# Performance work log

Measured on AMD Instinct MI355X. Metric: run time of the kernel, lower is better.

The kernel has to match this reference:

```python
import jax, jax.numpy as jnp
import numpy as np

L, N, B, S, H = 8, 4, 2, 4096, 256  # layers, sharers, batch, seq, hidden_dim
TAU = 0.5


def _mlp5(x, w1, b1, w2, b2):
    # x: [L,N,B,S,C], w1: [L,C,H], w2: [L,H,H] -> per-layer Linear-ReLU-Linear
    h = jax.nn.relu(jnp.einsum('lnbsc,lch->lnbsh', x, w1) + b1[:, None, None, None, :])
    return jnp.einsum('lnbsh,lhd->lnbsd', h, w2) + b2[:, None, None, None, :]


def _mlp4(x, w1, b1, w2, b2):
    # x: [L,B,S,C], w1: [L,C,H], w2: [L,H,H]
    h = jax.nn.relu(jnp.einsum('lbsc,lch->lbsh', x, w1) + b1[:, None, None, :])
    return jnp.einsum('lbsh,lhd->lbsd', h, w2) + b2[:, None, None, :]


def setup_inputs() -> dict:
    key = jax.random.key(0)
    ks = jax.random.split(key, 26)
    sc = 1.0 / np.sqrt(H)
    sc2 = 1.0 / np.sqrt(2 * H)
    d = {
        'receiver_k': jax.random.normal(ks[0], (L, B, S, H), jnp.float32),
        'receiver_v': jax.random.normal(ks[1], (L, B, S, H), jnp.float32),
        'sharer_k': jax.random.normal(ks[2], (L, N, B, S, H), jnp.float32),
        'sharer_v': jax.random.normal(ks[3], (L, N, B, S, H), jnp.float32),
        'edge_weights': jax.random.uniform(ks[4], (L, N), jnp.float32),
        'alpha': jnp.zeros((L,), jnp.float32),  # layer_gates_alpha init = zeros
        'ak_w1': jax.random.normal(ks[5], (L, H, H), jnp.float32) * sc,
        'ak_b1': jnp.zeros((L, H), jnp.float32),
        'ak_w2': jax.random.normal(ks[6], (L, H, H), jnp.float32) * sc,
        'ak_b2': jnp.zeros((L, H), jnp.float32),
        'av_w1': jax.random.normal(ks[7], (L, H, H), jnp.float32) * sc,
        'av_b1': jnp.zeros((L, H), jnp.float32),
        'av_w2': jax.random.normal(ks[8], (L, H, H), jnp.float32) * sc,
        'av_b2': jnp.zeros((L, H), jnp.float32),
        'fk_w1': jax.random.normal(ks[9], (L, 2 * H, H), jnp.float32) * sc2,
        'fk_b1': jnp.zeros((L, H), jnp.float32),
        'fk_w2': jax.random.normal(ks[10], (L, H, H), jnp.float32) * sc,
        'fk_b2': jnp.zeros((L, H), jnp.float32),
        'fv_w1': jax.random.normal(ks[11], (L, 2 * H, H), jnp.float32) * sc2,
        'fv_b1': jnp.zeros((L, H), jnp.float32),
        'fv_w2': jax.random.normal(ks[12], (L, H, H), jnp.float32) * sc,
        'fv_b2': jnp.zeros((L, H), jnp.float32),
    }
    return d


def reference(receiver_k, receiver_v, sharer_k, sharer_v, edge_weights, alpha,
              ak_w1, ak_b1, ak_w2, ak_b2, av_w1, av_b1, av_w2, av_b2,
              fk_w1, fk_b1, fk_w2, fk_b2, fv_w1, fv_b1, fv_w2, fv_b2):
    gate = jax.nn.sigmoid(alpha / TAU)[:, None, None, None]  # [L,1,1,1]
    # Align each sharer cache per layer
    aligned_k = _mlp5(sharer_k, ak_w1, ak_b1, ak_w2, ak_b2)
    aligned_v = _mlp5(sharer_v, av_w1, av_b1, av_w2, av_b2)
    # Weighted aggregation over sharers, divided by sharer count
    agg_k = jnp.einsum('ln,lnbsh->lbsh', edge_weights, aligned_k) / N
    agg_v = jnp.einsum('ln,lnbsh->lbsh', edge_weights, aligned_v) / N
    # Gated fusion with receiver cache
    delta_k = _mlp4(jnp.concatenate([receiver_k, agg_k], axis=-1), fk_w1, fk_b1, fk_w2, fk_b2)
    delta_v = _mlp4(jnp.concatenate([receiver_v, agg_v], axis=-1), fv_w1, fv_b1, fv_w2, fv_b2)
    fused_k = receiver_k + gate * delta_k
    fused_v = receiver_v + gate * delta_v
    return jnp.stack([fused_k, fused_v])  # [2,L,B,S,H]
```

## Files before the change

### kernel.cpp

```cpp
#include <hip/hip_runtime.h>
#include <hip/hip_bf16.h>


typedef unsigned int  u32;
typedef unsigned short u16;
typedef __attribute__((ext_vector_type(8))) short bf16x8;
typedef __attribute__((ext_vector_type(4))) float f32x4;

#define LL   8
#define NN   4
#define HH   256
#define RPL  8192
#define BM   64
#define ST   (BM * HH)

#define LSTRIDE 655360
#define O_AKW1 0
#define O_AKW2 65536
#define O_AVW1 131072
#define O_AVW2 196608
#define O_FKW1 262144
#define O_FKW2 393216
#define O_FVW1 458752
#define O_FVW2 589824

__device__ __forceinline__ u16 f2bf(float f) {
  return __builtin_bit_cast(u16, __float2bfloat16(f));
}
__device__ __forceinline__ float bf2f(u16 b) {
  u32 u = ((u32)b) << 16;
  return __builtin_bit_cast(float, u);
}
__device__ __forceinline__ float4 ldf4(const float* p) { return *(const float4*)p; }

__global__ __launch_bounds__(256) void prep_wt_k(
    const float* __restrict__ s0, const float* __restrict__ s1,
    const float* __restrict__ s2, const float* __restrict__ s3,
    const float* __restrict__ s4, const float* __restrict__ s5,
    const float* __restrict__ s6, const float* __restrict__ s7,
    u16* __restrict__ wt)
{
  __shared__ float tile[32][33];
  const int mat = blockIdx.z, l = blockIdx.y, t = blockIdx.x;
  const float* src; int off, K;
  switch (mat) {
    case 0: src = s0; off = O_AKW1; K = 256; break;
    case 1: src = s1; off = O_AKW2; K = 256; break;
    case 2: src = s2; off = O_AVW1; K = 256; break;
    case 3: src = s3; off = O_AVW2; K = 256; break;
    case 4: src = s4; off = O_FKW1; K = 512; break;
    case 5: src = s5; off = O_FKW2; K = 256; break;
    case 6: src = s6; off = O_FVW1; K = 512; break;
    default: src = s7; off = O_FVW2; K = 256; break;
  }
  const int ntk = K >> 5;
  if (t >= ntk * 8) return;
  const int tk = t % ntk, tp = t / ntk;
  src += (size_t)l * K * HH;
  u16* dst = wt + (size_t)l * LSTRIDE + off;
  #pragma unroll
  for (int i = 0; i < 4; ++i) {
    int idx = threadIdx.x + i * 256;
    int r = idx >> 5, c = idx & 31;
    tile[r][c] = src[(size_t)(tk * 32 + r) * HH + tp * 32 + c];
  }
  __syncthreads();
  const int pl = threadIdx.x >> 3, kq = threadIdx.x & 7;
  const int p = tp * 32 + pl;
  ushort4 o;
  o.x = f2bf(tile[kq * 4 + 0][pl]);
  o.y = f2bf(tile[kq * 4 + 1][pl]);
  o.z = f2bf(tile[kq * 4 + 2][pl]);
  o.w = f2bf(tile[kq * 4 + 3][pl]);
  *(ushort4*)(dst + (size_t)tk * 8192 + p * 32 + kq * 4) = o;
}

__device__ __forceinline__ void zero24(f32x4 (&a)[2][4]) {
  f32x4 z = {0.f, 0.f, 0.f, 0.f};
  #pragma unroll
  for (int i = 0; i < 2; ++i)
    #pragma unroll
    for (int j = 0; j < 4; ++j) a[i][j] = z;
}

__device__ __forceinline__ void stWrite(u16* dst, const float4& v, int idx) {
  int q = idx >> 6, c = (idx & 63) * 4;
  ushort4 o;
  o.x = f2bf(v.x); o.y = f2bf(v.y);
  o.z = f2bf(v.z); o.w = f2bf(v.w);
  *(ushort4*)(dst + q * HH + (c ^ ((q & 7) << 3))) = o;
}

template<bool STG>
__device__ __forceinline__ void gemm8R(
    f32x4 (&acc)[2][4], const bf16x8 (&ws)[16], const u16* __restrict__ act,
    const float* __restrict__ src, u16* __restrict__ dst,
    int tid, int lr, int g)
{
  float4 slot[8];
  if (STG) {
    #pragma unroll
    for (int c = 0; c < 8; ++c)
      slot[c] = ldf4(src + (size_t)(c * 512 + tid) * 4);
    __builtin_amdgcn_sched_barrier(0);
  }
  #pragma unroll
  for (int kt = 0; kt < 8; ++kt) {
    bf16x8 b[4];
    #pragma unroll
    for (int fq = 0; fq < 4; ++fq) {
      int q = fq * 16 + lr;
      int k = (kt * 32 + g * 8) ^ ((q & 7) << 3);
      b[fq] = *(const bf16x8*)(act + q * HH + k);
    }
    #pragma unroll
    for (int fp = 0; fp < 2; ++fp)
      #pragma unroll
      for (int fq = 0; fq < 4; ++fq)
        acc[fp][fq] = __builtin_amdgcn_mfma_f32_16x16x32_bf16(ws[kt * 2 + fp], b[fq], acc[fp][fq], 0, 0, 0);
  }
  if (STG) {
    __builtin_amdgcn_sched_barrier(0);
    #pragma unroll
    for (int c = 0; c < 8; ++c)
      stWrite(dst, slot[c], c * 512 + tid);
  }
}

template<bool STG>
__device__ __forceinline__ void gemm8S(
    f32x4 (&acc)[2][4], const u16* __restrict__ wtile, const u16* __restrict__ act,
    const float* __restrict__ src, u16* __restrict__ dst,
    int tid, int w, int lr, int g)
{
  const u16* wl = wtile + (w * 32 + lr) * 32 + g * 8;
  bf16x8 a[4][2];
  #pragma unroll
  for (int c = 0; c < 3; ++c)
    #pragma unroll
    for (int fp = 0; fp < 2; ++fp)
      a[c][fp] = *(const bf16x8*)(wl + c * 8192 + fp * 512);
  __builtin_amdgcn_sched_barrier(0x38F);
  float4 slot[8];
  if (STG) {
    #pragma unroll
    for (int c = 0; c < 8; ++c)
      slot[c] = ldf4(src + (size_t)(c * 512 + tid) * 4);
    __builtin_amdgcn_sched_barrier(0);
  }
  #pragma unroll
  for (int kt = 0; kt < 8; ++kt) {
    const int cur = kt & 3;
    if (kt < 5) {
      #pragma unroll
      for (int fp = 0; fp < 2; ++fp)
        a[(kt + 3) & 3][fp] = *(const bf16x8*)(wl + (kt + 3) * 8192 + fp * 512);
    }
    bf16x8 b[4];
    #pragma unroll
    for (int fq = 0; fq < 4; ++fq) {
      int q = fq * 16 + lr;
      int k = (kt * 32 + g * 8) ^ ((q & 7) << 3);
      b[fq] = *(const bf16x8*)(act + q * HH + k);
    }
    #pragma unroll
    for (int fp = 0; fp < 2; ++fp)
      #pragma unroll
      for (int fq = 0; fq < 4; ++fq)
        acc[fp][fq] = __builtin_amdgcn_mfma_f32_16x16x32_bf16(a[cur][fp], b[fq], acc[fp][fq], 0, 0, 0);
  }
  if (STG) {
    __builtin_amdgcn_sched_barrier(0);
    #pragma unroll
    for (int c = 0; c < 8; ++c)
      stWrite(dst, slot[c], c * 512 + tid);
  }
}

__device__ __forceinline__ void stageDirect(u16* dst, const float* __restrict__ src, int tid) {
  #pragma unroll
  for (int i = 0; i < 8; ++i) {
    float4 v = ldf4(src + (size_t)(i * 512 + tid) * 4);
    stWrite(dst, v, i * 512 + tid);
  }
}

template<bool INIT>
__device__ __forceinline__ void hsUpd(
    u16* HS, f32x4 (&acc)[2][4], const float* __restrict__ b1,
    float sn, int w, int lr, int g)
{
  #pragma unroll
  for (int fp = 0; fp < 2; ++fp) {
    int p0 = w * 32 + fp * 16 + g * 4;
    float4 bv = *(const float4*)(b1 + p0);
    #pragma unroll
    for (int fq = 0; fq < 4; ++fq) {
      int q = fq * 16 + lr;
      u16* addr = HS + q * HH + (p0 ^ ((q & 7) << 3));
      float v0 = sn * fmaxf(acc[fp][fq][0] + bv.x, 0.f);
      float v1 = sn * fmaxf(acc[fp][fq][1] + bv.y, 0.f);
      float v2 = sn * fmaxf(acc[fp][fq][2] + bv.z, 0.f);
      float v3 = sn * fmaxf(acc[fp][fq][3] + bv.w, 0.f);
      if (!INIT) {
        ushort4 old = *(ushort4*)addr;
        v0 += bf2f(old.x); v1 += bf2f(old.y);
        v2 += bf2f(old.z); v3 += bf2f(old.w);
      }
      ushort4 o;
      o.x = f2bf(v0); o.y = f2bf(v1);
      o.z = f2bf(v2); o.w = f2bf(v3);
      *(ushort4*)addr = o;
    }
  }
}

__device__ __forceinline__ void epiLds(
    u16* buf, f32x4 (&acc)[2][4], const float* __restrict__ bias,
    float bscale, bool doRelu, int w, int lr, int g)
{
  #pragma unroll
  for (int fp = 0; fp < 2; ++fp) {
    int p0 = w * 32 + fp * 16 + g * 4;
    float4 bv = *(const float4*)(bias + p0);
    #pragma unroll
    for (int fq = 0; fq < 4; ++fq) {
      int q = fq * 16 + lr;
      float v0 = acc[fp][fq][0] + bscale * bv.x;
      float v1 = acc[fp][fq][1] + bscale * bv.y;
      float v2 = acc[fp][fq][2] + bscale * bv.z;
      float v3 = acc[fp][fq][3] + bscale * bv.w;
      if (doRelu) {
        v0 = fmaxf(v0, 0.f); v1 = fmaxf(v1, 0.f);
        v2 = fmaxf(v2, 0.f); v3 = fmaxf(v3, 0.f);
      }
      ushort4 o;
      o.x = f2bf(v0); o.y = f2bf(v1);
      o.z = f2bf(v2); o.w = f2bf(v3);
      *(ushort4*)(buf + q * HH + (p0 ^ ((q & 7) << 3))) = o;
    }
  }
}

__device__ __forceinline__ void epiOut(
    f32x4 (&acc)[2][4], const float* __restrict__ bias,
    const float* __restrict__ recv, float* __restrict__ outp,
    float gate, int w, int lr, int g)
{
  #pragma unroll
  for (int fp = 0; fp < 2; ++fp) {
    int p0 = w * 32 + fp * 16 + g * 4;
    float4 bv = *(const float4*)(bias + p0);
    #pragma unroll
    for (int fq = 0; fq < 4; ++fq) {
      int q = fq * 16 + lr;
      float4 rv = *(const float4*)(recv + (size_t)q * HH + p0);
      float4 ov;
      ov.x = rv.x + gate * (acc[fp][fq][0] + bv.x);
      ov.y = rv.y + gate * (acc[fp][fq][1] + bv.y);
      ov.z = rv.z + gate * (acc[fp][fq][2] + bv.z);
      ov.w = rv.w + gate * (acc[fp][fq][3] + bv.w);
      *(float4*)(outp + (size_t)q * HH + p0) = ov;
    }
  }
}

__global__ __launch_bounds__(512) void CacheFuser_73873437491748_kernel(
    const float* __restrict__ recv_k, const float* __restrict__ recv_v,
    const float* __restrict__ shar_k, const float* __restrict__ shar_v,
    const float* __restrict__ ew, const float* __restrict__ alpha,
    const float* __restrict__ ak_b1, const float* __restrict__ ak_b2,
    const float* __restrict__ av_b1, const float* __restrict__ av_b2,
    const float* __restrict__ fk_b1, const float* __restrict__ fk_b2,
    const float* __restrict__ fv_b1, const float* __restrict__ fv_b2,
    const u16* __restrict__ wt, float* __restrict__ out)
{
  __shared__ u16 XA[ST];
  __shared__ u16 XB[ST];
  __shared__ u16 HS[ST];
  __shared__ u16 FB[ST];

  const int bid = blockIdx.x;
  const int l = bid & 7, t = bid >> 3;
  const int tid = threadIdx.x;
  const int w = tid >> 6, lane = tid & 63, lr = lane & 15, g = lane >> 4;

  const size_t row0 = (size_t)t * BM;
  const u16* lw = wt + (size_t)l * LSTRIDE;
  const float gate = 1.f / (1.f + __expf(-2.f * alpha[l]));
  const float* ewl = ew + l * NN;

  stageDirect(XA, shar_k + ((size_t)l * NN * RPL + row0) * HH, tid);

  #pragma unroll 1
  for (int path = 0; path < 2; ++path) {
    const float* recvB = (path ? recv_v : recv_k) + ((size_t)l * RPL + row0) * HH;
    const float* sharB = (path ? shar_v : shar_k) + ((size_t)l * NN * RPL + row0) * HH;
    const u16* W1  = lw + (path ? O_AVW1 : O_AKW1);
    const u16* W2  = lw + (path ? O_AVW2 : O_AKW2);
    const u16* FW1 = lw + (path ? O_FVW1 : O_FKW1);
    const u16* FW2 = lw + (path ? O_FVW2 : O_FKW2);
    const float* b1  = (path ? av_b1 : ak_b1) + l * HH;
    const float* b2  = (path ? av_b2 : ak_b2) + l * HH;
    const float* fb1 = (path ? fv_b1 : fk_b1) + l * HH;
    const float* fb2 = (path ? fv_b2 : fk_b2) + l * HH;
    float* outp = out + ((size_t)(path * LL + l) * RPL + row0) * HH;

    bf16x8 ws[16];
    {
      const u16* wl = W1 + (w * 32 + lr) * 32 + g * 8;
      #pragma unroll
      for (int kt = 0; kt < 8; ++kt)
        #pragma unroll
        for (int fp = 0; fp < 2; ++fp)
          ws[kt * 2 + fp] = *(const bf16x8*)(wl + kt * 8192 + fp * 512);
    }

    int cur = path;
    float sS = 0.f;

    #pragma unroll 1
    for (int n = 0; n < NN; ++n) {
      float sn = ewl[n] * 0.25f; sS += sn;
      __syncthreads();
      u16* XC = cur ? XB : XA;
      u16* XO = cur ? XA : XB;
      const float* nsrc = (n < 3) ? sharB + (size_t)(n + 1) * RPL * HH : recvB;
      f32x4 h[2][4]; zero24(h);
      gemm8R<true>(h, ws, XC, nsrc, XO, tid, lr, g);
      if (n == 0) hsUpd<true >(HS, h, b1, sn, w, lr, g);
      else        hsUpd<false>(HS, h, b1, sn, w, lr, g);
      cur ^= 1;
    }
    u16* XR = cur ? XB : XA;
    u16* XD = cur ? XA : XB;
    __syncthreads();
    f32x4 agg[2][4]; zero24(agg);
    gemm8S<false>(agg, W2, HS, nullptr, nullptr, tid, w, lr, g);
    epiLds(FB, agg, b2, sS, false, w, lr, g);
    __syncthreads();
    f32x4 h2[2][4]; zero24(h2);
    if (path == 0) {
      gemm8S<true>(h2, FW1, XR, shar_v + ((size_t)l * NN * RPL + row0) * HH, XD,
                   tid, w, lr, g);
    } else {
      gemm8S<false>(h2, FW1, XR, nullptr, nullptr, tid, w, lr, g);
    }
    gemm8S<false>(h2, FW1 + 8 * 8192, FB, nullptr, nullptr, tid, w, lr, g);
    epiLds(HS, h2, fb1, 1.f, true, w, lr, g);
    __syncthreads();
    f32x4 dd[2][4]; zero24(dd);
    gemm8S<false>(dd, FW2, HS, nullptr, nullptr, tid, w, lr, g);
    epiOut(dd, fb2, recvB, outp, gate, w, lr, g);
    cur ^= 1;
  }
}

extern "C" void kernel_launch(void* const* d_in, const int* in_sizes, int n_in,
                              void* d_out, int out_size, void* d_ws, size_t ws_size,
                              hipStream_t stream)
{
  const float* recv_k = (const float*)d_in[0];
  const float* recv_v = (const float*)d_in[1];
  const float* shar_k = (const float*)d_in[2];
  const float* shar_v = (const float*)d_in[3];
  const float* ew     = (const float*)d_in[4];
  const float* alpha  = (const float*)d_in[5];
  const float* ak_w1 = (const float*)d_in[6];  const float* ak_b1 = (const float*)d_in[7];
  const float* ak_w2 = (const float*)d_in[8];  const float* ak_b2 = (const float*)d_in[9];
  const float* av_w1 = (const float*)d_in[10]; const float* av_b1 = (const float*)d_in[11];
  const float* av_w2 = (const float*)d_in[12]; const float* av_b2 = (const float*)d_in[13];
  const float* fk_w1 = (const float*)d_in[14]; const float* fk_b1 = (const float*)d_in[15];
  const float* fk_w2 = (const float*)d_in[16]; const float* fk_b2 = (const float*)d_in[17];
  const float* fv_w1 = (const float*)d_in[18]; const float* fv_b1 = (const float*)d_in[19];
  const float* fv_w2 = (const float*)d_in[20]; const float* fv_b2 = (const float*)d_in[21];
  u16* wtw = (u16*)d_ws;
  float* outp = (float*)d_out;

  prep_wt_k<<<dim3(128, 8, 8), dim3(256), 0, stream>>>(
      ak_w1, ak_w2, av_w1, av_w2, fk_w1, fk_w2, fv_w1, fv_w2, wtw);

  CacheFuser_73873437491748_kernel<<<dim3(1024), dim3(512), 0, stream>>>(
      recv_k, recv_v, shar_k, shar_v, ew, alpha,
      ak_b1, ak_b2, av_b1, av_b2, fk_b1, fk_b2, fv_b1, fv_b2, wtw, outp);
}
```

Measured before the change: 256.0 us.

## Unroll both paths and merge GEMM phases to remove block barriers

Replaces the two-iteration path loop and the inner sharer loop with straight-line code. Independent GEMMs are merged between barriers: the W2 aggregation GEMM and the first half of the fusion FW1 GEMM now run in the same phase. The V-path first sharer GEMM and the next weight-register load now overlap with the K-path's final GEMM and output epilogue, with LDS buffers (HS/FB) swapped between paths to avoid hazards. The aim is fewer __syncthreads and more overlap. The cost is larger code and higher register pressure, since more accumulators are live at once.

```diff
diff --git a/kernel.cpp b/kernel.cpp
--- a/kernel.cpp
+++ b/kernel.cpp
@@ -89,6 +89,15 @@
   o.x = f2bf(v.x); o.y = f2bf(v.y);
   o.z = f2bf(v.z); o.w = f2bf(v.w);
   *(ushort4*)(dst + q * HH + (c ^ ((q & 7) << 3))) = o;
+}
+
+__device__ __forceinline__ void loadWS(bf16x8 (&ws)[16], const u16* W1, int w, int lr, int g) {
+  const u16* wl = W1 + (w * 32 + lr) * 32 + g * 8;
+  #pragma unroll
+  for (int kt = 0; kt < 8; ++kt)
+    #pragma unroll
+    for (int fp = 0; fp < 2; ++fp)
+      ws[kt * 2 + fp] = *(const bf16x8*)(wl + kt * 8192 + fp * 512);
 }
 
 template<bool STG>
@@ -289,71 +298,69 @@
   const u16* lw = wt + (size_t)l * LSTRIDE;
   const float gate = 1.f / (1.f + __expf(-2.f * alpha[l]));
   const float* ewl = ew + l * NN;
-
-  stageDirect(XA, shar_k + ((size_t)l * NN * RPL + row0) * HH, tid);
-
-  #pragma unroll 1
-  for (int path = 0; path < 2; ++path) {
-    const float* recvB = (path ? recv_v : recv_k) + ((size_t)l * RPL + row0) * HH;
-    const float* sharB = (path ? shar_v : shar_k) + ((size_t)l * NN * RPL + row0) * HH;
-    const u16* W1  = lw + (path ? O_AVW1 : O_AKW1);
-    const u16* W2  = lw + (path ? O_AVW2 : O_AKW2);
-    const u16* FW1 = lw + (path ? O_FVW1 : O_FKW1);
-    const u16* FW2 = lw + (path ? O_FVW2 : O_FKW2);
-    const float* b1  = (path ? av_b1 : ak_b1) + l * HH;
-    const float* b2  = (path ? av_b2 : ak_b2) + l * HH;
-    const float* fb1 = (path ? fv_b1 : fk_b1) + l * HH;
-    const float* fb2 = (path ? fv_b2 : fk_b2) + l * HH;
-    float* outp = out + ((size_t)(path * LL + l) * RPL + row0) * HH;
-
-    bf16x8 ws[16];
-    {
-      const u16* wl = W1 + (w * 32 + lr) * 32 + g * 8;
-      #pragma unroll
-      for (int kt = 0; kt < 8; ++kt)
-        #pragma unroll
-        for (int fp = 0; fp < 2; ++fp)
-          ws[kt * 2 + fp] = *(const bf16x8*)(wl + kt * 8192 + fp * 512);
-    }
-
-    int cur = path;
-    float sS = 0.f;
-
-    #pragma unroll 1
-    for (int n = 0; n < NN; ++n) {
-      float sn = ewl[n] * 0.25f; sS += sn;
-      __syncthreads();
-      u16* XC = cur ? XB : XA;
-      u16* XO = cur ? XA : XB;
-      const float* nsrc = (n < 3) ? sharB + (size_t)(n + 1) * RPL * HH : recvB;
-      f32x4 h[2][4]; zero24(h);
-      gemm8R<true>(h, ws, XC, nsrc, XO, tid, lr, g);
-      if (n == 0) hsUpd<true >(HS, h, b1, sn, w, lr, g);
-      else        hsUpd<false>(HS, h, b1, sn, w, lr, g);
-      cur ^= 1;
-    }
-    u16* XR = cur ? XB : XA;
-    u16* XD = cur ? XA : XB;
-    __syncthreads();
-    f32x4 agg[2][4]; zero24(agg);
-    gemm8S<false>(agg, W2, HS, nullptr, nullptr, tid, w, lr, g);
-    epiLds(FB, agg, b2, sS, false, w, lr, g);
-    __syncthreads();
-    f32x4 h2[2][4]; zero24(h2);
-    if (path == 0) {
-      gemm8S<true>(h2, FW1, XR, shar_v + ((size_t)l * NN * RPL + row0) * HH, XD,
-                   tid, w, lr, g);
-    } else {
-      gemm8S<false>(h2, FW1, XR, nullptr, nullptr, tid, w, lr, g);
-    }
-    gemm8S<false>(h2, FW1 + 8 * 8192, FB, nullptr, nullptr, tid, w, lr, g);
-    epiLds(HS, h2, fb1, 1.f, true, w, lr, g);
-    __syncthreads();
-    f32x4 dd[2][4]; zero24(dd);
-    gemm8S<false>(dd, FW2, HS, nullptr, nullptr, tid, w, lr, g);
-    epiOut(dd, fb2, recvB, outp, gate, w, lr, g);
-    cur ^= 1;
-  }
+  const float sn0 = ewl[0] * 0.25f, sn1 = ewl[1] * 0.25f;
+  const float sn2 = ewl[2] * 0.25f, sn3 = ewl[3] * 0.25f;
+  const float sS = sn0 + sn1 + sn2 + sn3;
+
+  const float* recvK = recv_k + ((size_t)l * RPL + row0) * HH;
+  const float* recvV = recv_v + ((size_t)l * RPL + row0) * HH;
+  const float* sharK = shar_k + ((size_t)l * NN * RPL + row0) * HH;
+  const float* sharV = shar_v + ((size_t)l * NN * RPL + row0) * HH;
+  float* outK = out + ((size_t)l * RPL + row0) * HH;
+  float* outV = out + (((size_t)LL + l) * RPL + row0) * HH;
+
+  stageDirect(XA, sharK, tid);
+
+  bf16x8 ws[16];
+  loadWS(ws, lw + O_AKW1, w, lr, g);
+
+  f32x4 h[2][4], agg[2][4], h2[2][4], dd[2][4];
+
+  __syncthreads();
+  zero24(h); gemm8R<true>(h, ws, XA, sharK + (size_t)1 * RPL * HH, XB, tid, lr, g);
+  hsUpd<true >(HS, h, ak_b1 + l * HH, sn0, w, lr, g);
+  __syncthreads();
+  zero24(h); gemm8R<true>(h, ws, XB, sharK + (size_t)2 * RPL * HH, XA, tid, lr, g);
+  hsUpd<false>(HS, h, ak_b1 + l * HH, sn1, w, lr, g);
+  __syncthreads();
+  zero24(h); gemm8R<true>(h, ws, XA, sharK + (size_t)3 * RPL * HH, XB, tid, lr, g);
+  hsUpd<false>(HS, h, ak_b1 + l * HH, sn2, w, lr, g);
+  __syncthreads();
+  zero24(h); gemm8R<true>(h, ws, XB, recvK, XA, tid, lr, g);
+  hsUpd<false>(HS, h, ak_b1 + l * HH, sn3, w, lr, g);
+  __syncthreads();
+  zero24(agg); gemm8S<false>(agg, lw + O_AKW2, HS, nullptr, nullptr, tid, w, lr, g);
+  zero24(h2);  gemm8S<true >(h2,  lw + O_FKW1, XA, sharV, XB, tid, w, lr, g);
+  epiLds(FB, agg, ak_b2 + l * HH, sS, false, w, lr, g);
+  __syncthreads();
+  gemm8S<false>(h2, lw + O_FKW1 + 8 * 8192, FB, nullptr, nullptr, tid, w, lr, g);
+  epiLds(HS, h2, fk_b1 + l * HH, 1.f, true, w, lr, g);
+  __syncthreads();
+  loadWS(ws, lw + O_AVW1, w, lr, g);
+  zero24(dd); gemm8S<false>(dd, lw + O_FKW2, HS, nullptr, nullptr, tid, w, lr, g);
+  epiOut(dd, fk_b2 + l * HH, recvK, outK, gate, w, lr, g);
+  zero24(h); gemm8R<true>(h, ws, XB, sharV + (size_t)1 * RPL * HH, XA, tid, lr, g);
+  hsUpd<true >(FB, h, av_b1 + l * HH, sn0, w, lr, g);
+
+  __syncthreads();
+  zero24(h); gemm8R<true>(h, ws, XA, sharV + (size_t)2 * RPL * HH, XB, tid, lr, g);
+  hsUpd<false>(FB, h, av_b1 + l * HH, sn1, w, lr, g);
+  __syncthreads();
+  zero24(h); gemm8R<true>(h, ws, XB, sharV + (size_t)3 * RPL * HH, XA, tid, lr, g);
+  hsUpd<false>(FB, h, av_b1 + l * HH, sn2, w, lr, g);
+  __syncthreads();
+  zero24(h); gemm8R<true>(h, ws, XA, recvV, XB, tid, lr, g);
+  hsUpd<false>(FB, h, av_b1 + l * HH, sn3, w, lr, g);
+  __syncthreads();
+  zero24(agg); gemm8S<false>(agg, lw + O_AVW2, FB, nullptr, nullptr, tid, w, lr, g);
+  zero24(h2);  gemm8S<false>(h2,  lw + O_FVW1, XB, nullptr, nullptr, tid, w, lr, g);
+  epiLds(HS, agg, av_b2 + l * HH, sS, false, w, lr, g);
+  __syncthreads();
+  gemm8S<false>(h2, lw + O_FVW1 + 8 * 8192, HS, nullptr, nullptr, tid, w, lr, g);
+  epiLds(FB, h2, fv_b1 + l * HH, 1.f, true, w, lr, g);
+  __syncthreads();
+  zero24(dd); gemm8S<false>(dd, lw + O_FVW2, FB, nullptr, nullptr, tid, w, lr, g);
+  epiOut(dd, fv_b2 + l * HH, recvV, outV, gate, w, lr, g);
 }
 
 extern "C" void kernel_launch(void* const* d_in, const int* in_sizes, int n_in,
```

Result: slower. 282.5 us (+10.4%).
